# Optimization experiments

Hardware: AMD Instinct MI355X
Metric: run time of the kernel (lower is better)

Reference implementation:

```python
import jax, jax.numpy as jnp
import numpy as np

K = 3          # kernel / stride
D = 32         # bond dimension
OUT = 10       # output classes
N_SITES = 27   # feature_dim after squeeze = C * k**3 = 27 -> sites per MPS


def squeeze_3d(img, k=K):
    # space-to-depth with channel sum, feature order (x,y,z) matching the
    # original nested-loop kernel extraction: feature = x*k*k + y*k + z
    H, V, Dd, C = img.shape
    x = img.reshape(H // k, k, V // k, k, Dd // k, k, C)
    x = x.transpose(0, 2, 4, 1, 3, 5, 6).sum(-1)  # (nH,nV,nD,k,k,k)
    return x.reshape(H // k, V // k, Dd // k, k ** 3)


def embed_trig(x):
    # trigonometric embedding, phys_dim = 2
    a = (jnp.pi / 2.0) * x
    return jnp.stack([jnp.cos(a), jnp.sin(a)], axis=-1)


def mps_chain(first, mid, last, e):
    # Batched tensor-train (SMPO with one output leg on site 0) contraction.
    # first: (N,2,O,D)   site 0, phys leg 2, output leg O, right bond D
    # mid:   (N,M,D,2,D) sites 1..n-2
    # last:  (N,D,2)     site n-1
    # e:     (N,n,2)     embedded inputs
    v0 = jnp.einsum('npod,np->nod', first, e[:, 0])              # (N,O,D)
    mats = jnp.einsum('nmdpe,nmp->nmde', mid, e[:, 1:-1])        # (N,M,D,D)

    def step(v, M):
        return jnp.einsum('nod,nde->noe', v, M), None

    v, _ = jax.lax.scan(step, v0, jnp.moveaxis(mats, 1, 0))
    return jnp.einsum('nod,ndp,np->no', v, last, e[:, -1])       # (N,O)


def unsqueeze_3d(v):
    # (N, feat) -> (s,s,s,1) with mean over feature dim
    n, f = v.shape
    s = round(n ** (1.0 / 3.0))
    return v.reshape(s, s, s, f).mean(-1, keepdims=True)


def setup_inputs():
    key = jax.random.key(0)
    ks = jax.random.split(key, 10)
    scale = 1.0 / np.sqrt(D)  # keeps 27-site matrix chain numerically stable
    mk = lambda k, sh: jax.random.normal(k, sh, dtype=jnp.float32) * scale
    n = N_SITES
    return {
        'input_image': jax.random.uniform(ks[0], (27, 27, 27, 1), dtype=jnp.float32),
        'l0_first': mk(ks[1], (729, 2, 1, D)),
        'l0_mid':   mk(ks[2], (729, n - 2, D, 2, D)),
        'l0_last':  mk(ks[3], (729, D, 2)),
        'l1_first': mk(ks[4], (27, 2, 1, D)),
        'l1_mid':   mk(ks[5], (27, n - 2, D, 2, D)),
        'l1_last':  mk(ks[6], (27, D, 2)),
        'f_first':  mk(ks[7], (2, OUT, D)),
        'f_mid':    mk(ks[8], (n - 2, D, 2, D)),
        'f_last':   mk(ks[9], (D, 2)),
    }


def reference(input_image, l0_first, l0_mid, l0_last,
              l1_first, l1_mid, l1_last, f_first, f_mid, f_last):
    # Layer 0: (27,27,27,1) -> squeeze (9,9,9,27) -> 729 MPS contractions
    sq = squeeze_3d(input_image).reshape(729, N_SITES)
    out0 = mps_chain(l0_first, l0_mid, l0_last, embed_trig(sq))   # (729,1)
    x = unsqueeze_3d(out0)                                        # (9,9,9,1)

    # Layer 1: (9,9,9,1) -> squeeze (3,3,3,27) -> 27 MPS contractions
    sq = squeeze_3d(x).reshape(27, N_SITES)
    out1 = mps_chain(l1_first, l1_mid, l1_last, embed_trig(sq))   # (27,1)
    x = unsqueeze_3d(out1)                                        # (3,3,3,1)

    # Final layer: (3,3,3,1) -> squeeze (1,1,1,27) -> one MPS with output leg
    sq = squeeze_3d(x).reshape(1, N_SITES)
    out = mps_chain(f_first[None], f_mid[None], f_last[None], embed_trig(sq))
    return out.reshape(OUT)
```

## Files before the change

### kernel.cpp

```cpp
#include <hip/hip_runtime.h>
#include <math.h>

#define NSITES 27
#define NMID   25
#define DD     32

#define FENCE asm volatile("s_waitcnt lgkmcnt(0)" ::: "memory");

#define LOADB(BUF, S)                                                   \
    {                                                                   \
        const float4* pm_ = m4 + (size_t)(S) * 512;                     \
        _Pragma("unroll")                                               \
        for (int k = 0; k < 8; ++k) BUF[k] = pm_[64 * k];               \
    }

#define COMPUTE(BUF, EI)                                                \
    {                                                                   \
        FENCE                                                           \
        const float e0_ = sE[EI][0];                                    \
        const float e1_ = sE[EI][1];                                    \
        float4 acc; acc.x = acc.y = acc.z = acc.w = 0.f;                \
        _Pragma("unroll")                                               \
        for (int k = 0; k < 8; ++k) {                                   \
            const float vd = sV[dbase + 4 * k];                         \
            acc.x = fmaf(BUF[k].x, vd, acc.x);                          \
            acc.y = fmaf(BUF[k].y, vd, acc.y);                          \
            acc.z = fmaf(BUF[k].z, vd, acc.z);                          \
            acc.w = fmaf(BUF[k].w, vd, acc.w);                          \
        }                                                               \
        _Pragma("unroll")                                               \
        for (int mask = 16; mask <= 32; mask <<= 1) {                   \
            acc.x += __shfl_xor(acc.x, mask, 64);                       \
            acc.y += __shfl_xor(acc.y, mask, 64);                       \
            acc.z += __shfl_xor(acc.z, mask, 64);                       \
            acc.w += __shfl_xor(acc.w, mask, 64);                       \
        }                                                               \
        float4 oth;                                                     \
        oth.x = __shfl_xor(acc.x, 8, 64);                               \
        oth.y = __shfl_xor(acc.y, 8, 64);                               \
        oth.z = __shfl_xor(acc.z, 8, 64);                               \
        oth.w = __shfl_xor(acc.w, 8, 64);                               \
        const float cm = p ? e1_ : e0_;                                 \
        const float co = p ? e0_ : e1_;                                 \
        float4 nv;                                                      \
        nv.x = fmaf(cm, acc.x, co * oth.x);                             \
        nv.y = fmaf(cm, acc.y, co * oth.y);                             \
        nv.z = fmaf(cm, acc.z, co * oth.z);                             \
        nv.w = fmaf(cm, acc.w, co * oth.w);                             \
        if (lane < 8) sV4[lane] = nv;                                   \
    }

__global__ __launch_bounds__(64) void mps_layer_kernel(
    const float* __restrict__ src,
    const float* __restrict__ first,
    const float* __restrict__ mid,
    const float* __restrict__ last,
    float*       __restrict__ out,
    int B, int nChains)
{
    const int lane = threadIdx.x;
    const int n = blockIdx.x;
    if (n >= nChains) return;

    __shared__ float  sE[NSITES][2];
    __shared__ float4 sV4[8];
    float* sV = (float*)sV4;

    const int S = 3 * B;
    const int bh = n / (B * B);
    const int bv = (n / B) % B;
    const int bd = n % B;

    if (lane < NSITES) {
        const int kh = lane / 9, kv = (lane / 3) % 3, kd = lane % 3;
        const float x = src[(size_t)(bh*3 + kh) * S * S + (bv*3 + kv) * S + (bd*3 + kd)];
        float sn, cs;
        sincosf(1.5707963267948966f * x, &sn, &cs);
        sE[lane][0] = cs;
        sE[lane][1] = sn;
    }
    FENCE
    if (lane < DD) {
        const float* f = first + (size_t)n * (2 * DD);
        sV[lane] = fmaf(f[lane], sE[0][0], f[DD + lane] * sE[0][1]);
    }

    const int p     = (lane >> 3) & 1;
    const int dbase = lane >> 4;
    const float4* m4 = (const float4*)(mid + (size_t)n * NMID * 2048) + lane;

    float4 q0[8], q1[8], q2[8], q3[8], q4[8];
    LOADB(q0, 0)
    LOADB(q1, 1)
    LOADB(q2, 2)
    LOADB(q3, 3)
    LOADB(q4, 4)

    for (int m = 0; m < NMID; m += 5) {
        COMPUTE(q0, m + 1)
        if (m + 5 < NMID) LOADB(q0, m + 5)
        COMPUTE(q1, m + 2)
        if (m + 6 < NMID) LOADB(q1, m + 6)
        COMPUTE(q2, m + 3)
        if (m + 7 < NMID) LOADB(q2, m + 7)
        COMPUTE(q3, m + 4)
        if (m + 8 < NMID) LOADB(q3, m + 8)
        COMPUTE(q4, m + 5)
        if (m + 9 < NMID) LOADB(q4, m + 9)
    }
    FENCE

    const float le0 = sE[26][0], le1 = sE[26][1];
    float tacc = 0.f;
    if (lane < DD) {
        const float* L = last + (size_t)n * (DD * 2);
        tacc = sV[lane] * fmaf(L[2 * lane], le0, L[2 * lane + 1] * le1);
    }
#pragma unroll
    for (int mask = 1; mask < 64; mask <<= 1) tacc += __shfl_xor(tacc, mask, 64);
    if (lane == 0) out[n] = tacc;
}

#define FSITE(BUF, M)                                                   \
    {                                                                   \
        FENCE                                                           \
        const float e0_ = sE[(M) + 1][0];                               \
        const float e1_ = sE[(M) + 1][1];                               \
        const float ep_ = p ? e1_ : e0_;                                \
        const float4 u4 = ((const float4*)sU)[e4];                      \
        const float wx = ep_ * u4.x, wy = ep_ * u4.y;                   \
        const float wz = ep_ * u4.z, ww = ep_ * u4.w;                   \
        float acc[8];                                                   \
        _Pragma("unroll")                                               \
        for (int k = 0; k < 8; ++k) {                                   \
            const float4 Mv = BUF[k];                                   \
            acc[k] = fmaf(Mv.x, wx, fmaf(Mv.y, wy, fmaf(Mv.z, wz, Mv.w * ww))); \
        }                                                               \
        _Pragma("unroll")                                               \
        for (int mask = 1; mask <= 8; mask <<= 1) {                     \
            _Pragma("unroll")                                           \
            for (int k = 0; k < 8; ++k) acc[k] += __shfl_xor(acc[k], mask, 64); \
        }                                                               \
        if ((lane & 15) == 0) {                                         \
            _Pragma("unroll")                                           \
            for (int k = 0; k < 8; ++k) sU[dbase + 4 * k] = acc[k];     \
        }                                                               \
    }

__global__ __launch_bounds__(64) void mps_final_kernel(
    const float* __restrict__ x,
    const float* __restrict__ ffirst,
    const float* __restrict__ fmid,
    const float* __restrict__ flast,
    float*       __restrict__ out)
{
    const int lane = threadIdx.x;
    __shared__ float sE[NSITES][2];
    __shared__ float sU[DD];

    if (lane < NSITES) {
        float sn, cs;
        sincosf(1.5707963267948966f * x[lane], &sn, &cs);
        sE[lane][0] = cs;
        sE[lane][1] = sn;
    }
    FENCE
    if (lane < DD) {
        sU[lane] = fmaf(flast[2 * lane], sE[26][0], flast[2 * lane + 1] * sE[26][1]);
    }

    const int p     = (lane >> 3) & 1;
    const int e4    = lane & 7;
    const int dbase = lane >> 4;
    const float4* m4 = (const float4*)fmid + lane;

    float4 c0[8], c1[8], c2[8], c3[8], c4[8];
    LOADB(c0, 24)
    LOADB(c1, 23)
    LOADB(c2, 22)
    LOADB(c3, 21)
    LOADB(c4, 20)

    for (int t = 0; t < 5; ++t) {
        const int s0 = 24 - 5 * t;
        FSITE(c0, s0)
        if (s0 - 5 >= 0) LOADB(c0, s0 - 5)
        FSITE(c1, s0 - 1)
        if (s0 - 6 >= 0) LOADB(c1, s0 - 6)
        FSITE(c2, s0 - 2)
        if (s0 - 7 >= 0) LOADB(c2, s0 - 7)
        FSITE(c3, s0 - 3)
        if (s0 - 8 >= 0) LOADB(c3, s0 - 8)
        FSITE(c4, s0 - 4)
        if (s0 - 9 >= 0) LOADB(c4, s0 - 9)
    }
    FENCE

    const float e0 = sE[0][0], e1 = sE[0][1];
    const float ud = (lane < DD) ? sU[lane] : 0.f;
#pragma unroll
    for (int o = 0; o < 10; ++o) {
        float t = 0.f;
        if (lane < DD)
            t = fmaf(ffirst[o * DD + lane], e0, ffirst[320 + o * DD + lane] * e1) * ud;
#pragma unroll
        for (int mask = 1; mask < 64; mask <<= 1) t += __shfl_xor(t, mask, 64);
        if (lane == 0) out[o] = t;
    }
}

extern "C" void kernel_launch(void* const* d_in, const int* in_sizes, int n_in,
                              void* d_out, int out_size, void* d_ws, size_t ws_size,
                              hipStream_t stream) {
    const float* img = (const float*)d_in[0];
    const float* l0f = (const float*)d_in[1];
    const float* l0m = (const float*)d_in[2];
    const float* l0l = (const float*)d_in[3];
    const float* l1f = (const float*)d_in[4];
    const float* l1m = (const float*)d_in[5];
    const float* l1l = (const float*)d_in[6];
    const float* ff  = (const float*)d_in[7];
    const float* fm  = (const float*)d_in[8];
    const float* fl  = (const float*)d_in[9];
    float* out  = (float*)d_out;
    float* out0 = (float*)d_ws;
    float* out1 = out0 + 729;

    mps_layer_kernel<<<729, 64, 0, stream>>>(img,  l0f, l0m, l0l, out0, 9, 729);
    mps_layer_kernel<<<27,  64, 0, stream>>>(out0, l1f, l1m, l1l, out1, 3, 27);
    mps_final_kernel<<<1,   64, 0, stream>>>(out1, ff,  fm,  fl,  out);
}
```

Baseline: 271.1 us.

## Replace shared-memory state exchange with wavefront shuffles in MPS chain kernels

Moves the per-step bond vector and the embedding coefficients out of LDS and into registers, broadcasting them with __shfl. This removes the per-site LDS write/read and the lgkmcnt fences between sites. The mid-tensor prefetch is also issued before the embedding sincos and src loads, so those overlap with the memory loads. The trade-off is more cross-lane shuffle instructions and register pressure per site, and the lane-mapping logic is more intricate.

```diff
diff --git a/kernel.cpp b/kernel.cpp
--- a/kernel.cpp
+++ b/kernel.cpp
@@ -5,8 +5,6 @@
 #define NMID   25
 #define DD     32
 
-#define FENCE asm volatile("s_waitcnt lgkmcnt(0)" ::: "memory");
-
 #define LOADB(BUF, S)                                                   \
     {                                                                   \
         const float4* pm_ = m4 + (size_t)(S) * 512;                     \
@@ -16,17 +14,15 @@
 
 #define COMPUTE(BUF, EI)                                                \
     {                                                                   \
-        FENCE                                                           \
-        const float e0_ = sE[EI][0];                                    \
-        const float e1_ = sE[EI][1];                                    \
+        const float e0_ = __shfl(myCs, (EI), 64);                       \
+        const float e1_ = __shfl(mySn, (EI), 64);                       \
         float4 acc; acc.x = acc.y = acc.z = acc.w = 0.f;                \
         _Pragma("unroll")                                               \
         for (int k = 0; k < 8; ++k) {                                   \
-            const float vd = sV[dbase + 4 * k];                         \
-            acc.x = fmaf(BUF[k].x, vd, acc.x);                          \
-            acc.y = fmaf(BUF[k].y, vd, acc.y);                          \
-            acc.z = fmaf(BUF[k].z, vd, acc.z);                          \
-            acc.w = fmaf(BUF[k].w, vd, acc.w);                          \
+            acc.x = fmaf(BUF[k].x, vd[k], acc.x);                       \
+            acc.y = fmaf(BUF[k].y, vd[k], acc.y);                       \
+            acc.z = fmaf(BUF[k].z, vd[k], acc.z);                       \
+            acc.w = fmaf(BUF[k].w, vd[k], acc.w);                       \
         }                                                               \
         _Pragma("unroll")                                               \
         for (int mask = 16; mask <= 32; mask <<= 1) {                   \
@@ -47,7 +43,11 @@
         nv.y = fmaf(cm, acc.y, co * oth.y);                             \
         nv.z = fmaf(cm, acc.z, co * oth.z);                             \
         nv.w = fmaf(cm, acc.w, co * oth.w);                             \
-        if (lane < 8) sV4[lane] = nv;                                   \
+        sel = (dbase == 0) ? nv.x : (dbase == 1) ? nv.y                 \
+            : (dbase == 2) ? nv.z : nv.w;                               \
+        _Pragma("unroll")                                               \
+        for (int k = 0; k < 8; ++k)                                     \
+            vd[k] = __shfl(sel, selbase | k, 64);                       \
     }
 
 __global__ __launch_bounds__(64) void mps_layer_kernel(
@@ -62,31 +62,9 @@
     const int n = blockIdx.x;
     if (n >= nChains) return;
 
-    __shared__ float  sE[NSITES][2];
-    __shared__ float4 sV4[8];
-    float* sV = (float*)sV4;
-
-    const int S = 3 * B;
-    const int bh = n / (B * B);
-    const int bv = (n / B) % B;
-    const int bd = n % B;
-
-    if (lane < NSITES) {
-        const int kh = lane / 9, kv = (lane / 3) % 3, kd = lane % 3;
-        const float x = src[(size_t)(bh*3 + kh) * S * S + (bv*3 + kv) * S + (bd*3 + kd)];
-        float sn, cs;
-        sincosf(1.5707963267948966f * x, &sn, &cs);
-        sE[lane][0] = cs;
-        sE[lane][1] = sn;
-    }
-    FENCE
-    if (lane < DD) {
-        const float* f = first + (size_t)n * (2 * DD);
-        sV[lane] = fmaf(f[lane], sE[0][0], f[DD + lane] * sE[0][1]);
-    }
-
-    const int p     = (lane >> 3) & 1;
-    const int dbase = lane >> 4;
+    const int p       = (lane >> 3) & 1;
+    const int dbase   = lane >> 4;
+    const int selbase = lane & 56;
     const float4* m4 = (const float4*)(mid + (size_t)n * NMID * 2048) + lane;
 
     float4 q0[8], q1[8], q2[8], q3[8], q4[8];
@@ -95,6 +73,29 @@
     LOADB(q2, 2)
     LOADB(q3, 3)
     LOADB(q4, 4)
+
+    const int S = 3 * B;
+    const int bh = n / (B * B);
+    const int bv = (n / B) % B;
+    const int bd = n % B;
+    float myCs, mySn;
+    {
+        const int s  = lane < NSITES ? lane : NSITES - 1;
+        const int kh = s / 9, kv = (s / 3) % 3, kd = s % 3;
+        const float x = src[(size_t)(bh*3 + kh) * S * S + (bv*3 + kv) * S + (bd*3 + kd)];
+        sincosf(1.5707963267948966f * x, &mySn, &myCs);
+    }
+
+    const float cs0 = __shfl(myCs, 0, 64);
+    const float sn0 = __shfl(mySn, 0, 64);
+    const float* f = first + (size_t)n * (2 * DD);
+    float vd[8];
+    float sel;
+#pragma unroll
+    for (int k = 0; k < 8; ++k) {
+        const int d = dbase + 4 * k;
+        vd[k] = fmaf(f[d], cs0, f[DD + d] * sn0);
+    }
 
     for (int m = 0; m < NMID; m += 5) {
         COMPUTE(q0, m + 1)
@@ -108,13 +109,14 @@
         COMPUTE(q4, m + 5)
         if (m + 9 < NMID) LOADB(q4, m + 9)
     }
-    FENCE
-
-    const float le0 = sE[26][0], le1 = sE[26][1];
+
+    const float le0 = __shfl(myCs, 26, 64);
+    const float le1 = __shfl(mySn, 26, 64);
+    const float vL  = __shfl(sel, ((lane & 3) << 4) | ((lane & 31) >> 2), 64);
     float tacc = 0.f;
     if (lane < DD) {
         const float* L = last + (size_t)n * (DD * 2);
-        tacc = sV[lane] * fmaf(L[2 * lane], le0, L[2 * lane + 1] * le1);
+        tacc = vL * fmaf(L[2 * lane], le0, L[2 * lane + 1] * le1);
     }
 #pragma unroll
     for (int mask = 1; mask < 64; mask <<= 1) tacc += __shfl_xor(tacc, mask, 64);
@@ -123,11 +125,9 @@
 
 #define FSITE(BUF, M)                                                   \
     {                                                                   \
-        FENCE                                                           \
-        const float e0_ = sE[(M) + 1][0];                               \
-        const float e1_ = sE[(M) + 1][1];                               \
+        const float e0_ = __shfl(myCs, (M) + 1, 64);                    \
+        const float e1_ = __shfl(mySn, (M) + 1, 64);                    \
         const float ep_ = p ? e1_ : e0_;                                \
-        const float4 u4 = ((const float4*)sU)[e4];                      \
         const float wx = ep_ * u4.x, wy = ep_ * u4.y;                   \
         const float wz = ep_ * u4.z, ww = ep_ * u4.w;                   \
         float acc[8];                                                   \
@@ -141,10 +141,19 @@
             _Pragma("unroll")                                           \
             for (int k = 0; k < 8; ++k) acc[k] += __shfl_xor(acc[k], mask, 64); \
         }                                                               \
-        if ((lane & 15) == 0) {                                         \
-            _Pragma("unroll")                                           \
-            for (int k = 0; k < 8; ++k) sU[dbase + 4 * k] = acc[k];     \
-        }                                                               \
+        {                                                               \
+            const float t01 = (e4 & 1) ? acc[1] : acc[0];               \
+            const float t23 = (e4 & 1) ? acc[3] : acc[2];               \
+            const float t45 = (e4 & 1) ? acc[5] : acc[4];               \
+            const float t67 = (e4 & 1) ? acc[7] : acc[6];               \
+            const float t03 = (e4 & 2) ? t23 : t01;                     \
+            const float t47 = (e4 & 2) ? t67 : t45;                     \
+            usel = (e4 & 4) ? t47 : t03;                                \
+        }                                                               \
+        u4.x = __shfl(usel, (lane & 15),      64);                      \
+        u4.y = __shfl(usel, (lane & 15) | 16, 64);                      \
+        u4.z = __shfl(usel, (lane & 15) | 32, 64);                      \
+        u4.w = __shfl(usel, (lane & 15) | 48, 64);                      \
     }
 
 __global__ __launch_bounds__(64) void mps_final_kernel(
@@ -155,23 +164,8 @@
     float*       __restrict__ out)
 {
     const int lane = threadIdx.x;
-    __shared__ float sE[NSITES][2];
-    __shared__ float sU[DD];
-
-    if (lane < NSITES) {
-        float sn, cs;
-        sincosf(1.5707963267948966f * x[lane], &sn, &cs);
-        sE[lane][0] = cs;
-        sE[lane][1] = sn;
-    }
-    FENCE
-    if (lane < DD) {
-        sU[lane] = fmaf(flast[2 * lane], sE[26][0], flast[2 * lane + 1] * sE[26][1]);
-    }
-
     const int p     = (lane >> 3) & 1;
     const int e4    = lane & 7;
-    const int dbase = lane >> 4;
     const float4* m4 = (const float4*)fmid + lane;
 
     float4 c0[8], c1[8], c2[8], c3[8], c4[8];
@@ -180,6 +174,24 @@
     LOADB(c2, 22)
     LOADB(c3, 21)
     LOADB(c4, 20)
+
+    float myCs, mySn;
+    {
+        const int s = lane < NSITES ? lane : NSITES - 1;
+        sincosf(1.5707963267948966f * x[s], &mySn, &myCs);
+    }
+
+    const float cs26 = __shfl(myCs, 26, 64);
+    const float sn26 = __shfl(mySn, 26, 64);
+    float4 u4;
+    {
+        const int d0 = 4 * e4;
+        u4.x = fmaf(flast[2*d0    ], cs26, flast[2*d0 + 1] * sn26);
+        u4.y = fmaf(flast[2*d0 + 2], cs26, flast[2*d0 + 3] * sn26);
+        u4.z = fmaf(flast[2*d0 + 4], cs26, flast[2*d0 + 5] * sn26);
+        u4.w = fmaf(flast[2*d0 + 6], cs26, flast[2*d0 + 7] * sn26);
+    }
+    float usel;
 
     for (int t = 0; t < 5; ++t) {
         const int s0 = 24 - 5 * t;
@@ -194,10 +206,11 @@
         FSITE(c4, s0 - 4)
         if (s0 - 9 >= 0) LOADB(c4, s0 - 9)
     }
-    FENCE
-
-    const float e0 = sE[0][0], e1 = sE[0][1];
-    const float ud = (lane < DD) ? sU[lane] : 0.f;
+
+    const float ud0 = __shfl(usel, ((lane & 3) << 4) | ((lane & 31) >> 2), 64);
+    const float e0 = __shfl(myCs, 0, 64);
+    const float e1 = __shfl(mySn, 0, 64);
+    const float ud = (lane < DD) ? ud0 : 0.f;
 #pragma unroll
     for (int o = 0; o < 10; ++o) {
         float t = 0.f;
```

Result: no change. 269.1 us (-0.8%).
